# Performance work log

Hardware: AMD Instinct MI355X
Metric: run time of the kernel (lower is better)

The kernel has to match this reference:

```python
import jax, jax.numpy as jnp
import numpy as np

N_LAYERS = 8
D_MODEL = 64
D_STATE = 32
D_CONV = 4
D_INNER = 128          # expand * d_model
HEADDIM = 64
NHEADS = D_INNER // HEADDIM      # 2
CONV_DIM = D_INNER + 2 * D_STATE # 192 (x, B, C)
D_IN_PROJ = 2 * D_INNER + 2 * D_STATE + NHEADS  # 322
EPS = 1e-5


def setup_inputs() -> dict:
    key = jax.random.key(0)
    ks = jax.random.split(key, 8)
    x = jax.random.normal(ks[0], (16, 4096, D_MODEL), dtype=jnp.float32)
    Win = jax.random.normal(ks[1], (N_LAYERS, D_MODEL, D_IN_PROJ), dtype=jnp.float32) * 0.05
    conv_w = jax.random.normal(ks[2], (N_LAYERS, CONV_DIM, D_CONV), dtype=jnp.float32) * 0.2
    conv_b = jnp.zeros((N_LAYERS, CONV_DIM), dtype=jnp.float32)
    dt_bias = jax.random.uniform(ks[3], (N_LAYERS, NHEADS), minval=-4.0, maxval=-1.0)
    A_log = jnp.log(jax.random.uniform(ks[4], (N_LAYERS, NHEADS), minval=1.0, maxval=16.0))
    Dp = jnp.ones((N_LAYERS, NHEADS), dtype=jnp.float32)
    norm_w = jnp.ones((N_LAYERS, D_INNER), dtype=jnp.float32)
    Wout = jax.random.normal(ks[5], (N_LAYERS, D_INNER, D_MODEL), dtype=jnp.float32) * 0.05
    return {"x": x, "Win": Win, "conv_w": conv_w, "conv_b": conv_b,
            "dt_bias": dt_bias, "A_log": A_log, "Dp": Dp,
            "norm_w": norm_w, "Wout": Wout}


def _mamba2_layer(u, Win, conv_w, conv_b, dt_bias, A_log, Dp, norm_w, Wout):
    b, l, _ = u.shape
    zxbcdt = u @ Win                                   # (b,l,322)
    z = zxbcdt[..., :D_INNER]                          # gate (b,l,128)
    xBC = zxbcdt[..., D_INNER:D_INNER + CONV_DIM]      # (b,l,192)
    dt = jax.nn.softplus(zxbcdt[..., D_INNER + CONV_DIM:] + dt_bias)  # (b,l,H)

    # causal depthwise conv over time, then SiLU
    xc = jnp.pad(xBC.transpose(0, 2, 1), ((0, 0), (0, 0), (D_CONV - 1, 0)))
    xc = jax.lax.conv_general_dilated(
        xc, conv_w[:, None, :], (1,), 'VALID',
        feature_group_count=CONV_DIM,
        dimension_numbers=('NCH', 'OIH', 'NCH'))
    xBC = jax.nn.silu((xc + conv_b[None, :, None]).transpose(0, 2, 1))  # (b,l,192)

    xs = xBC[..., :D_INNER].reshape(b, l, NHEADS, HEADDIM)   # (b,l,h,p)
    B = xBC[..., D_INNER:D_INNER + D_STATE]                  # (b,l,n)
    C = xBC[..., D_INNER + D_STATE:]                         # (b,l,n)

    A = -jnp.exp(A_log)                                      # (h,) negative
    dA = jnp.exp(dt * A)                                     # (b,l,h)

    # sequential selective scan over time; state (b,h,p,n)
    def step(hst, inp):
        dA_t, dt_t, x_t, B_t, C_t = inp
        hst = hst * dA_t[:, :, None, None] + \
              (dt_t[:, :, None] * x_t)[..., None] * B_t[:, None, None, :]
        y_t = jnp.einsum('bhpn,bn->bhp', hst, C_t)
        return hst, y_t

    h0 = jnp.zeros((b, NHEADS, HEADDIM, D_STATE), dtype=u.dtype)
    seq = (jnp.moveaxis(dA, 1, 0), jnp.moveaxis(dt, 1, 0),
           jnp.moveaxis(xs, 1, 0), jnp.moveaxis(B, 1, 0), jnp.moveaxis(C, 1, 0))
    _, ys = jax.lax.scan(step, h0, seq)                      # (l,b,h,p)
    y = jnp.moveaxis(ys, 0, 1) + Dp[None, None, :, None] * xs  # (b,l,h,p)
    y = y.reshape(b, l, D_INNER)

    # gated RMSNorm (norm_before_gate=False): normalize after gating
    y = y * jax.nn.silu(z)
    y = y * jax.lax.rsqrt(jnp.mean(y * y, axis=-1, keepdims=True) + EPS) * norm_w
    return y @ Wout                                          # (b,l,d_model)


def reference(x, Win, conv_w, conv_b, dt_bias, A_log, Dp, norm_w, Wout):
    h = x
    for i in range(N_LAYERS - 1):
        h = _mamba2_layer(h, Win[i], conv_w[i], conv_b[i], dt_bias[i],
                          A_log[i], Dp[i], norm_w[i], Wout[i])
    h = jax.lax.stop_gradient(h)  # layers[:-1] run under torch.no_grad()
    i = N_LAYERS - 1
    return _mamba2_layer(h, Win[i], conv_w[i], conv_b[i], dt_bias[i],
                         A_log[i], Dp[i], norm_w[i], Wout[i])
```

## Files before the change

kernel.cpp:

```cpp
#include <hip/hip_runtime.h>
#include <math.h>

#define BATCH   16
#define SEQ     4096
#define DMODEL  64
#define DINNER  128
#define DSTATE  32
#define NHEADS  2
#define HEADDIM 64
#define CONVDIM 192
#define PROJ    322
#define QC      64
#define NCHUNK  (SEQ/QC)
#define BL      (BATCH*SEQ)
#define NPAD    336

typedef __attribute__((ext_vector_type(8))) short short8;
typedef __attribute__((ext_vector_type(4))) float f32x4;

__device__ inline unsigned short f2b(float f){
  union { float f; unsigned u; } v; v.f = f;
  unsigned r = v.u + 0x7FFF + ((v.u >> 16) & 1);
  return (unsigned short)(r >> 16);
}
__device__ inline float b2f(unsigned short s){
  union { unsigned u; float f; } v; v.u = ((unsigned)s) << 16; return v.f;
}
__device__ inline void split2(float x, unsigned short& h, unsigned short& l){
  unsigned short hh = f2b(x);
  h = hh;
  l = f2b(x - b2f(hh));
}

__device__ float g_z   [(size_t)BL*DINNER];
__device__ float g_xbc [(size_t)BL*CONVDIM];
__device__ float g_y   [(size_t)BL*DINNER];
__device__ unsigned short g_C[(size_t)BL*DSTATE];
__device__ float g_dt  [BATCH*NHEADS*SEQ];
__device__ float g_cum [BATCH*NHEADS*SEQ];
__device__ float g_ctot[BATCH*NHEADS*NCHUNK];
__device__ float g_S   [BATCH*NHEADS*NCHUNK*DSTATE*HEADDIM];
__device__ float g_H   [BATCH*NHEADS*NCHUNK*DSTATE*HEADDIM];
__device__ float g_ping0[(size_t)BL*DMODEL];
__device__ float g_ping1[(size_t)BL*DMODEL];
__device__ unsigned short g_WinTh [8*NPAD*DMODEL];
__device__ unsigned short g_WinTl [8*NPAD*DMODEL];
__device__ unsigned short g_WoutTh[8*DMODEL*DINNER];
__device__ unsigned short g_WoutTl[8*DMODEL*DINNER];

__global__ __launch_bounds__(256) void k_prep(const float* __restrict__ Win,
                                              const float* __restrict__ Wout,
                                              const float* __restrict__ normw) {
  const int idx = blockIdx.x*256 + threadIdx.x;
  const int NW = 8*NPAD*DMODEL;
  if (idx < NW) {
    int layer = idx / (NPAD*DMODEL);
    int rem   = idx - layer*(NPAD*DMODEL);
    int n = rem >> 6, k = rem & 63;
    float v = (n < PROJ) ? Win[(size_t)layer*DMODEL*PROJ + k*PROJ + n] : 0.f;
    split2(v, g_WinTh[idx], g_WinTl[idx]);
  } else {
    int i2 = idx - NW;
    if (i2 < 8*DMODEL*DINNER) {
      int layer = i2 / (DMODEL*DINNER);
      int rem   = i2 - layer*(DMODEL*DINNER);
      int n = rem >> 7, k = rem & 127;
      float v = Wout[(size_t)layer*DINNER*DMODEL + k*DMODEL + n] * normw[layer*DINNER + k];
      split2(v, g_WoutTh[i2], g_WoutTl[i2]);
    }
  }
}

__global__ __launch_bounds__(256) void k_inproj(const float* __restrict__ xext, int sel,
                                                const unsigned short* __restrict__ WinTh,
                                                const unsigned short* __restrict__ WinTl,
                                                const float* __restrict__ Win,
                                                const float* __restrict__ dt_bias,
                                                const float* __restrict__ A_log) {
  __shared__ unsigned short Xhl[2][64][72];
  const float* __restrict__ X = (sel==0) ? xext : (sel==1 ? g_ping0 : g_ping1);
  const int bx = blockIdx.x;
  const int row0 = bx * 64;
  const int tid = threadIdx.x;
#pragma unroll
  for (int j=0;j<4;j++){
    int e = tid + j*256; int r = e>>4, c4 = (e&15)*4;
    float4 v = *(const float4*)&X[(size_t)(row0+r)*DMODEL + c4];
    split2(v.x, Xhl[0][r][c4+0], Xhl[1][r][c4+0]);
    split2(v.y, Xhl[0][r][c4+1], Xhl[1][r][c4+1]);
    split2(v.z, Xhl[0][r][c4+2], Xhl[1][r][c4+2]);
    split2(v.w, Xhl[0][r][c4+3], Xhl[1][r][c4+3]);
  }
  const int w = tid>>6, l = tid&63, lane15 = l&15, quad = l>>4;
  if (w < 2) {
    const int h = w, t = l;
    float acc = 0.f;
    const float* xr = &X[(size_t)(row0+t)*DMODEL];
#pragma unroll
    for (int k=0;k<64;k++) acc = fmaf(xr[k], Win[k*PROJ + (DINNER+CONVDIM) + h], acc);
    float xv = acc + dt_bias[h];
    float dtv = (xv > 20.f) ? xv : log1pf(expf(xv));
    float A = -expf(A_log[h]);
    float cum = dtv * A;
#pragma unroll
    for (int off=1; off<64; off<<=1){
      float v = __shfl_up(cum, off);
      if (t >= off) cum += v;
    }
    const int b = bx>>6, ch = bx&63;
    const int base = (b*NHEADS + h)*SEQ + ch*QC + t;
    g_dt [base] = dtv;
    g_cum[base] = cum;
    if (t == 63) g_ctot[(b*NHEADS+h)*NCHUNK + ch] = cum;
  }
  __syncthreads();
  short8 a0h = *(const short8*)&Xhl[0][16*w + lane15][quad*8];
  short8 a1h = *(const short8*)&Xhl[0][16*w + lane15][quad*8 + 32];
  short8 a0l = *(const short8*)&Xhl[1][16*w + lane15][quad*8];
  short8 a1l = *(const short8*)&Xhl[1][16*w + lane15][quad*8 + 32];
  __syncthreads();
  float (*stg)[68] = (float(*)[68])((float*)&Xhl[0][0][0] + (size_t)w*16*68);
#pragma unroll 1
  for (int g5=0; g5<5; g5++){
    f32x4 acc4[4];
#pragma unroll
    for (int tt=0; tt<4; tt++){
      int t = g5*4 + tt;
      const unsigned short* bph = &WinTh[(16*t + lane15)*64 + quad*8];
      const unsigned short* bpl = &WinTl[(16*t + lane15)*64 + quad*8];
      short8 b0h = *(const short8*)bph;
      short8 b1h = *(const short8*)(bph + 32);
      short8 b0l = *(const short8*)bpl;
      short8 b1l = *(const short8*)(bpl + 32);
      f32x4 acc = {0.f,0.f,0.f,0.f};
      acc = __builtin_amdgcn_mfma_f32_16x16x32_bf16(a0h, b0h, acc, 0, 0, 0);
      acc = __builtin_amdgcn_mfma_f32_16x16x32_bf16(a1h, b1h, acc, 0, 0, 0);
      acc = __builtin_amdgcn_mfma_f32_16x16x32_bf16(a0l, b0h, acc, 0, 0, 0);
      acc = __builtin_amdgcn_mfma_f32_16x16x32_bf16(a1l, b1h, acc, 0, 0, 0);
      acc = __builtin_amdgcn_mfma_f32_16x16x32_bf16(a0h, b0l, acc, 0, 0, 0);
      acc = __builtin_amdgcn_mfma_f32_16x16x32_bf16(a1h, b1l, acc, 0, 0, 0);
      acc4[tt] = acc;
    }
#pragma unroll
    for (int tt=0; tt<4; tt++)
#pragma unroll
      for (int r=0;r<4;r++)
        stg[quad*4+r][tt*16+lane15] = acc4[tt][r];
#pragma unroll
    for (int it=0; it<4; it++){
      int e = it*64 + l;
      int lr = e>>4, c4 = (e&15)<<2;
      float4 v = *(const float4*)&stg[lr][c4];
      size_t grow = row0 + 16*w + lr;
      int gcol = g5*64 + c4;
      if (g5 < 2) *(float4*)&g_z  [grow*DINNER  + gcol]          = v;
      else        *(float4*)&g_xbc[grow*CONVDIM + gcol - DINNER] = v;
    }
  }
}

__global__ __launch_bounds__(256,4) void k_chunkA(const float* __restrict__ conv_w,
                                                  const float* __restrict__ conv_b,
                                                  const float* __restrict__ Dp) {
  __shared__ float Xf[64][66];
  __shared__ unsigned short Xt [64][72];
  __shared__ unsigned short Bt [32][72];
  union BCG {
    struct { unsigned short Bsh[64][40]; unsigned short Csh[64][40]; } bc;
    unsigned short Gsh[64][72];
  };
  __shared__ BCG u;
  const int bx = blockIdx.x; const int b = bx>>7, h=(bx>>6)&1, ch=bx&63;
  const int tid = threadIdx.x;
  const size_t row0 = (size_t)b*SEQ + (size_t)ch*QC;
  const int cbase = (b*NHEADS+h)*SEQ + ch*QC;
  const float dph = Dp[h];
  if (tid < QC){
    float cl = g_cum[cbase+63];
    float cu = g_cum[cbase+tid], dtv = g_dt[cbase+tid];
    Xf[tid][64] = cu;
    Xf[tid][65] = dtv;
    ((float*)&Bt[tid>>1][64])[tid&1] = expf(cl - cu) * dtv;
  }
  const int cc = tid & 127, half = tid >> 7, t0 = half*32;
  const int gch = (cc < 64) ? (h*64 + cc) : (64 + cc);
  const float w0 = conv_w[gch*4+0], w1 = conv_w[gch*4+1], w2 = conv_w[gch*4+2], w3 = conv_w[gch*4+3];
  const float bb = conv_b[gch];
  float v0, v1, v2;
  if (ch==0 && half==0){ v0=0.f; v1=0.f; v2=0.f; }
  else {
    v0 = g_xbc[(row0+t0-3)*CONVDIM + gch];
    v1 = g_xbc[(row0+t0-2)*CONVDIM + gch];
    v2 = g_xbc[(row0+t0-1)*CONVDIM + gch];
  }
  __syncthreads();
  if (cc < 64){
#pragma unroll
    for (int blk=0; blk<4; ++blk){
      unsigned short xb[8];
#pragma unroll
      for (int j=0;j<8;j++){
        int t = t0 + blk*8 + j;
        float v3 = g_xbc[(row0+t)*CONVDIM + gch];
        float a = fmaf(w0,v0, fmaf(w1,v1, fmaf(w2,v2, fmaf(w3,v3, bb))));
        float sv = a / (1.f + expf(-a));
        Xf[cc][t] = sv;
        xb[j] = f2b(sv);
        v0=v1; v1=v2; v2=v3;
      }
      *(short8*)&Xt[cc][t0 + blk*8] = *(const short8*)xb;
    }
  } else if (cc < 96){
    const int n = cc - 64;
#pragma unroll
    for (int blk=0; blk<4; ++blk){
      unsigned short bt8[8];
#pragma unroll
      for (int j=0;j<8;j++){
        int t = t0 + blk*8 + j;
        float v3 = g_xbc[(row0+t)*CONVDIM + gch];
        float a = fmaf(w0,v0, fmaf(w1,v1, fmaf(w2,v2, fmaf(w3,v3, bb))));
        float sv = a / (1.f + expf(-a));
        u.bc.Bsh[t][n] = f2b(sv);
        float ew = ((const float*)&Bt[t>>1][64])[t&1];
        bt8[j] = f2b(sv * ew);
        v0=v1; v1=v2; v2=v3;
      }
      *(short8*)&Bt[n][t0 + blk*8] = *(const short8*)bt8;
    }
  } else {
    const int n = cc - 96;
#pragma unroll 4
    for (int t=t0; t<t0+32; t++){
      float v3 = g_xbc[(row0+t)*CONVDIM + gch];
      float a = fmaf(w0,v0, fmaf(w1,v1, fmaf(w2,v2, fmaf(w3,v3, bb))));
      float sv = a / (1.f + expf(-a));
      u.bc.Csh[t][n] = f2b(sv);
      if (h == 0) g_C[(row0+t)*DSTATE + n] = f2b(sv);
      v0=v1; v1=v2; v2=v3;
    }
  }
  __syncthreads();
  const int w = tid>>6, l = tid&63, lane15 = l&15, quad = l>>4;
  short8 afr = *(const short8*)&u.bc.Csh[16*w + lane15][quad*8];
  f32x4 gacc[4];
#pragma unroll
  for (int tn=0;tn<4;tn++){
    short8 bfr = *(const short8*)&u.bc.Bsh[16*tn + lane15][quad*8];
    f32x4 z = {0.f,0.f,0.f,0.f};
    gacc[tn] = __builtin_amdgcn_mfma_f32_16x16x32_bf16(afr, bfr, z, 0, 0, 0);
  }
  __syncthreads();
#pragma unroll
  for (int tn=0;tn<4;tn++){
    int s = 16*tn + lane15;
    float cs = Xf[s][64], ds = Xf[s][65];
#pragma unroll
    for (int r=0;r<4;r++){
      int t = 16*w + quad*4 + r;
      float gv = 0.f;
      if (s <= t) gv = expf(Xf[t][64]-cs) * ds * gacc[tn][r];
      u.Gsh[t][s] = f2b(gv);
    }
  }
  __syncthreads();
#pragma unroll
  for (int tn=0;tn<4;tn++){
    f32x4 acc = {0.f,0.f,0.f,0.f};
#pragma unroll
    for (int ks=0;ks<2;ks++){
      short8 a  = *(const short8*)&u.Gsh[16*w  + lane15][quad*8 + 32*ks];
      short8 bf = *(const short8*)&Xt [16*tn + lane15][quad*8 + 32*ks];
      acc = __builtin_amdgcn_mfma_f32_16x16x32_bf16(a, bf, acc, 0, 0, 0);
    }
    int p = 16*tn + lane15;
#pragma unroll
    for (int r=0;r<4;r++){
      int t = 16*w + quad*4 + r;
      g_y[(row0+t)*DINNER + h*HEADDIM + p] = acc[r] + dph * Xf[p][t];
    }
  }
  const size_t sb = (size_t)((b*NHEADS+h)*NCHUNK + ch) * (DSTATE*HEADDIM);
  const int tm2 = w & 1, tnb = (w>>1)*2;
#pragma unroll
  for (int tt=0;tt<2;tt++){
    int tn2 = tnb + tt;
    f32x4 acc = {0.f,0.f,0.f,0.f};
#pragma unroll
    for (int ks=0;ks<2;ks++){
      short8 a  = *(const short8*)&Bt[16*tm2 + lane15][quad*8 + 32*ks];
      short8 bf = *(const short8*)&Xt[16*tn2 + lane15][quad*8 + 32*ks];
      acc = __builtin_amdgcn_mfma_f32_16x16x32_bf16(a, bf, acc, 0, 0, 0);
    }
    int p = 16*tn2 + lane15;
#pragma unroll
    for (int r=0;r<4;r++){
      int n = 16*tm2 + quad*4 + r;
      g_S[sb + n*HEADDIM + p] = acc[r];
    }
  }
}

__global__ __launch_bounds__(256) void k_chunkScan() {
  __shared__ float dAc[NCHUNK];
  const int idx = blockIdx.x*256 + threadIdx.x;
  const int np = idx & 2047;
  const int bh = idx >> 11;
  if (threadIdx.x < NCHUNK) dAc[threadIdx.x] = expf(g_ctot[bh*NCHUNK + threadIdx.x]);
  __syncthreads();
  float h = 0.f;
  const size_t base = (size_t)bh*NCHUNK*2048 + np;
#pragma unroll 1
  for (int k0=0; k0<NCHUNK; k0+=8){
    float s[8];
#pragma unroll
    for (int j=0;j<8;j++) s[j] = g_S[base + (size_t)(k0+j)*2048];
    float hs[8];
#pragma unroll
    for (int j=0;j<8;j++){
      hs[j] = h;
      h = h*dAc[k0+j] + s[j];
    }
#pragma unroll
    for (int j=0;j<8;j++) g_H[base + (size_t)(k0+j)*2048] = hs[j];
  }
}

__global__ __launch_bounds__(256,3) void k_fusedC(const unsigned short* __restrict__ WoutTh,
                                                  const unsigned short* __restrict__ WoutTl,
                                                  float* __restrict__ dout, int dsel) {
  __shared__ float Cl[QC][DSTATE+1];
  __shared__ float ec[NHEADS][QC];
  __shared__ unsigned short yAh[64][136];
  __shared__ unsigned short yAl[64][136];
  float* __restrict__ out = (dsel==0) ? g_ping0 : (dsel==1 ? g_ping1 : dout);
  const int bx = blockIdx.x; const int b = bx>>6, ch = bx&63;
  const int tid = threadIdx.x;
  const size_t row0 = (size_t)b*SEQ + (size_t)ch*QC;
  const int w = tid>>6, l = tid&63, lane15 = l&15, quad = l>>4;
#pragma unroll
  for (int j=0;j<8;j++){ int e=tid+j*256; int s=e>>5, n=e&31;
    Cl[s][n] = b2f(g_C[(row0+s)*DSTATE + n]); }
  if (tid < 128){ int h_=tid>>6, s=tid&63;
    ec[h_][s] = expf(g_cum[(b*NHEADS+h_)*SEQ + ch*QC + s]); }
  float hr[64];
  {
    const float* H0 = &g_H[(size_t)((b*NHEADS+0)*NCHUNK + ch)*2048];
    const float* H1 = &g_H[(size_t)((b*NHEADS+1)*NCHUNK + ch)*2048];
#pragma unroll
    for (int n=0;n<32;n++){ hr[n] = H0[n*64 + l]; hr[32+n] = H1[n*64 + l]; }
  }
  __syncthreads();
#pragma unroll 1
  for (int i=0;i<16;i++){
    const int r = 16*w + i;
    const size_t row = row0 + r;
    float d0 = 0.f, d1 = 0.f;
#pragma unroll
    for (int n=0;n<32;n++){
      float c = Cl[r][n];
      d0 = fmaf(c, hr[n],    d0);
      d1 = fmaf(c, hr[32+n], d1);
    }
    float yv0 = g_y[row*DINNER + l]      + ec[0][r]*d0;
    float yv1 = g_y[row*DINNER + l + 64] + ec[1][r]*d1;
    float z0 = g_z[row*DINNER + l];
    float z1 = g_z[row*DINNER + l + 64];
    yv0 *= z0 / (1.f + expf(-z0));
    yv1 *= z1 / (1.f + expf(-z1));
    float ss = yv0*yv0 + yv1*yv1;
#pragma unroll
    for (int off=32; off>=1; off>>=1) ss += __shfl_xor(ss, off);
    float sc = rsqrtf(ss*(1.f/128.f) + 1e-5f);
    split2(yv0*sc, yAh[r][l],    yAl[r][l]);
    split2(yv1*sc, yAh[r][l+64], yAl[r][l+64]);
  }
  __syncthreads();
  short8 afh[4], afl[4];
#pragma unroll
  for (int ks=0;ks<4;ks++){
    afh[ks] = *(const short8*)&yAh[16*w + lane15][quad*8 + 32*ks];
    afl[ks] = *(const short8*)&yAl[16*w + lane15][quad*8 + 32*ks];
  }
  __syncthreads();
  float (*stgF)[68] = (float(*)[68])((float*)&yAh[0][0] + (size_t)w*16*68);
#pragma unroll
  for (int tc=0;tc<4;tc++){
    f32x4 acc = {0.f,0.f,0.f,0.f};
#pragma unroll
    for (int ks=0;ks<4;ks++){
      const unsigned short* bph = &WoutTh[(16*tc + lane15)*DINNER + quad*8 + 32*ks];
      const unsigned short* bpl = &WoutTl[(16*tc + lane15)*DINNER + quad*8 + 32*ks];
      short8 bh  = *(const short8*)bph;
      short8 blo = *(const short8*)bpl;
      acc = __builtin_amdgcn_mfma_f32_16x16x32_bf16(afh[ks], bh,  acc, 0, 0, 0);
      acc = __builtin_amdgcn_mfma_f32_16x16x32_bf16(afl[ks], bh,  acc, 0, 0, 0);
      acc = __builtin_amdgcn_mfma_f32_16x16x32_bf16(afh[ks], blo, acc, 0, 0, 0);
    }
#pragma unroll
    for (int r=0;r<4;r++)
      stgF[quad*4+r][tc*16+lane15] = acc[r];
  }
#pragma unroll
  for (int it=0; it<4; it++){
    int e = it*64 + l;
    int lr = e>>4, c4 = (e&15)<<2;
    float4 v = *(const float4*)&stgF[lr][c4];
    *(float4*)&out[(row0 + 16*w + lr)*DMODEL + c4] = v;
  }
}

extern "C" void kernel_launch(void* const* d_in, const int* in_sizes, int n_in,
                              void* d_out, int out_size, void* d_ws, size_t ws_size,
                              hipStream_t stream) {
  (void)in_sizes; (void)n_in; (void)d_ws; (void)ws_size; (void)out_size;
  const float* x       = (const float*)d_in[0];
  const float* Win     = (const float*)d_in[1];
  const float* conv_w  = (const float*)d_in[2];
  const float* conv_b  = (const float*)d_in[3];
  const float* dt_bias = (const float*)d_in[4];
  const float* A_log   = (const float*)d_in[5];
  const float* Dp      = (const float*)d_in[6];
  const float* norm_w  = (const float*)d_in[7];
  const float* Wout    = (const float*)d_in[8];

  k_prep<<<(8*(NPAD*DMODEL + DMODEL*DINNER) + 255)/256, 256, 0, stream>>>(Win, Wout, norm_w);

  unsigned short *winTh, *winTl, *woutTh, *woutTl;
  hipGetSymbolAddress((void**)&winTh,  HIP_SYMBOL(g_WinTh));
  hipGetSymbolAddress((void**)&winTl,  HIP_SYMBOL(g_WinTl));
  hipGetSymbolAddress((void**)&woutTh, HIP_SYMBOL(g_WoutTh));
  hipGetSymbolAddress((void**)&woutTl, HIP_SYMBOL(g_WoutTl));

  for (int layer = 0; layer < 8; ++layer) {
    const int insel = (layer==0) ? 0 : ((((layer-1)&1)==0) ? 1 : 2);
    const int dsel  = (layer==7) ? 2 : ((layer&1)==0 ? 0 : 1);

    k_inproj<<<BL/64, 256, 0, stream>>>(x, insel,
                                        winTh + (size_t)layer*NPAD*DMODEL,
                                        winTl + (size_t)layer*NPAD*DMODEL,
                                        Win + (size_t)layer*DMODEL*PROJ,
                                        dt_bias + layer*NHEADS, A_log + layer*NHEADS);
    k_chunkA<<<BATCH*NHEADS*NCHUNK, 256, 0, stream>>>(conv_w + (size_t)layer*CONVDIM*4,
                                                      conv_b + (size_t)layer*CONVDIM,
                                                      Dp + layer*NHEADS);
    k_chunkScan<<<(BATCH*NHEADS*DSTATE*HEADDIM)/256, 256, 0, stream>>>();
    k_fusedC<<<BATCH*NCHUNK, 256, 0, stream>>>(woutTh + (size_t)layer*DMODEL*DINNER,
                                               woutTl + (size_t)layer*DMODEL*DINNER,
                                               (float*)d_out, dsel);
  }
}
```

Baseline: 1.241 ms.

## Split in-projection across two blocks per chunk and load A fragments directly

The in-projection kernel now launches two blocks per 64-row chunk, each computing a subset of the output column groups (2 and 3 of 5), with only the first half computing dt and the cumulative decay. The A operand fragments are loaded straight from global memory into registers and split into hi/lo bf16 there, removing the shared-memory staging and two barriers. This doubles parallelism and cuts the per-block critical path. In exchange each chunk's input rows are read twice and the work split between the halves is uneven.

```diff
diff --git a/kernel.cpp b/kernel.cpp
--- a/kernel.cpp
+++ b/kernel.cpp
@@ -77,22 +77,21 @@
                                                 const float* __restrict__ Win,
                                                 const float* __restrict__ dt_bias,
                                                 const float* __restrict__ A_log) {
-  __shared__ unsigned short Xhl[2][64][72];
+  __shared__ float stgAll[4][16][68];
   const float* __restrict__ X = (sel==0) ? xext : (sel==1 ? g_ping0 : g_ping1);
   const int bx = blockIdx.x;
-  const int row0 = bx * 64;
+  const int chunk = bx >> 1, half = bx & 1;
+  const int row0 = chunk * 64;
   const int tid = threadIdx.x;
-#pragma unroll
-  for (int j=0;j<4;j++){
-    int e = tid + j*256; int r = e>>4, c4 = (e&15)*4;
-    float4 v = *(const float4*)&X[(size_t)(row0+r)*DMODEL + c4];
-    split2(v.x, Xhl[0][r][c4+0], Xhl[1][r][c4+0]);
-    split2(v.y, Xhl[0][r][c4+1], Xhl[1][r][c4+1]);
-    split2(v.z, Xhl[0][r][c4+2], Xhl[1][r][c4+2]);
-    split2(v.w, Xhl[0][r][c4+3], Xhl[1][r][c4+3]);
-  }
   const int w = tid>>6, l = tid&63, lane15 = l&15, quad = l>>4;
-  if (w < 2) {
+
+  const float* xrow = &X[(size_t)(row0 + 16*w + lane15)*DMODEL + quad*8];
+  float4 f0 = *(const float4*)(xrow);
+  float4 f1 = *(const float4*)(xrow + 4);
+  float4 f2 = *(const float4*)(xrow + 32);
+  float4 f3 = *(const float4*)(xrow + 36);
+
+  if (half==0 && w < 2) {
     const int h = w, t = l;
     float acc = 0.f;
     const float* xr = &X[(size_t)(row0+t)*DMODEL];
@@ -107,21 +106,29 @@
       float v = __shfl_up(cum, off);
       if (t >= off) cum += v;
     }
-    const int b = bx>>6, ch = bx&63;
+    const int b = chunk>>6, ch = chunk&63;
     const int base = (b*NHEADS + h)*SEQ + ch*QC + t;
     g_dt [base] = dtv;
     g_cum[base] = cum;
     if (t == 63) g_ctot[(b*NHEADS+h)*NCHUNK + ch] = cum;
   }
-  __syncthreads();
-  short8 a0h = *(const short8*)&Xhl[0][16*w + lane15][quad*8];
-  short8 a1h = *(const short8*)&Xhl[0][16*w + lane15][quad*8 + 32];
-  short8 a0l = *(const short8*)&Xhl[1][16*w + lane15][quad*8];
-  short8 a1l = *(const short8*)&Xhl[1][16*w + lane15][quad*8 + 32];
-  __syncthreads();
-  float (*stg)[68] = (float(*)[68])((float*)&Xhl[0][0][0] + (size_t)w*16*68);
+
+  short8 a0h, a0l, a1h, a1l;
+  {
+    float v0[8] = {f0.x,f0.y,f0.z,f0.w,f1.x,f1.y,f1.z,f1.w};
+    float v1[8] = {f2.x,f2.y,f2.z,f2.w,f3.x,f3.y,f3.z,f3.w};
+    unsigned short hh, ll;
+#pragma unroll
+    for (int j=0;j<8;j++){ split2(v0[j], hh, ll); a0h[j]=(short)hh; a0l[j]=(short)ll; }
+#pragma unroll
+    for (int j=0;j<8;j++){ split2(v1[j], hh, ll); a1h[j]=(short)hh; a1l[j]=(short)ll; }
+  }
+
+  float (*stg)[68] = stgAll[w];
+  const int gS = (half==0) ? 0 : 2;
+  const int gE = (half==0) ? 2 : 5;
 #pragma unroll 1
-  for (int g5=0; g5<5; g5++){
+  for (int g5=gS; g5<gE; g5++){
     f32x4 acc4[4];
 #pragma unroll
     for (int tt=0; tt<4; tt++){
@@ -436,7 +443,7 @@
     const int insel = (layer==0) ? 0 : ((((layer-1)&1)==0) ? 1 : 2);
     const int dsel  = (layer==7) ? 2 : ((layer&1)==0 ? 0 : 1);
 
-    k_inproj<<<BL/64, 256, 0, stream>>>(x, insel,
+    k_inproj<<<(BL/64)*2, 256, 0, stream>>>(x, insel,
                                         winTh + (size_t)layer*NPAD*DMODEL,
                                         winTl + (size_t)layer*NPAD*DMODEL,
                                         Win + (size_t)layer*DMODEL*PROJ,
```

Result: slower. 1.275 ms (+2.7%).
